# Kernel tuning notes

Hardware: AMD Instinct MI355X
Metric: run time of the kernel (lower is better)

## Reference

```python
import jax, jax.numpy as jnp
import numpy as np
import math

B, S, E = 2, 2048, 1024
NH, NKV, HD = 16, 4, 64
GATE_CH = 12

def _rope(x, cos, sin):
    h = x.shape[-1] // 2
    x1, x2 = x[..., :h], x[..., h:]
    return jnp.concatenate((x1 * cos + x2 * sin, x1 * -sin + x2 * cos), axis=-1)

def _rms_norm(x):
    eps = jnp.finfo(x.dtype).eps
    return x * jax.lax.rsqrt(jnp.mean(x * x, axis=-1, keepdims=True) + eps)

def setup_inputs() -> dict:
    key = jax.random.key(0)
    ks = jax.random.split(key, 9)
    x = jax.random.normal(ks[0], (B, S, E), dtype=jnp.float32)
    ve = jax.random.normal(ks[1], (B, S, NKV * HD), dtype=jnp.float32)
    t = jnp.arange(S, dtype=jnp.float32)[:, None]
    inv_freq = 1.0 / (10000.0 ** (jnp.arange(0, HD // 2, dtype=jnp.float32) / (HD // 2)))
    ang = t * inv_freq[None, :]
    cos = jnp.cos(ang)[None, :, None, :]  # (1,S,1,HD//2)
    sin = jnp.sin(ang)[None, :, None, :]
    attn_mask = jnp.tril(jnp.ones((S, S), dtype=bool))[None, None]  # causal (1,1,S,S)
    sc = 0.02
    Wq = jax.random.normal(ks[2], (NH * HD, E), dtype=jnp.float32) * sc
    Wk = jax.random.normal(ks[3], (NKV * HD, E), dtype=jnp.float32) * sc
    Wv = jax.random.normal(ks[4], (NKV * HD, E), dtype=jnp.float32) * sc
    Wproj = jax.random.normal(ks[5], (E, E), dtype=jnp.float32) * sc
    Wgate = jax.random.normal(ks[6], (NKV, GATE_CH), dtype=jnp.float32) * sc
    return {"x": x, "ve": ve, "cos": cos, "sin": sin, "attn_mask": attn_mask,
            "Wq": Wq, "Wk": Wk, "Wv": Wv, "Wproj": Wproj, "Wgate": Wgate}

def reference(x, ve, cos, sin, attn_mask, Wq, Wk, Wv, Wproj, Wgate):
    b, s, _ = x.shape
    q = (x @ Wq.T).reshape(b, s, NH, HD)
    k = (x @ Wk.T).reshape(b, s, NKV, HD)
    v = (x @ Wv.T).reshape(b, s, NKV, HD)
    # value-embedding gating
    gate = 3.0 * jax.nn.sigmoid(x[..., :GATE_CH] @ Wgate.T)  # (b,s,NKV)
    v = v + gate[..., None] * ve.reshape(b, s, NKV, HD)
    # RoPE + QK-RMSNorm
    q = _rms_norm(_rope(q, cos, sin)) * 1.2
    k = _rms_norm(_rope(k, cos, sin)) * 1.2
    # GQA: repeat KV heads
    rep = NH // NKV
    k = jnp.repeat(k, rep, axis=2)
    v = jnp.repeat(v, rep, axis=2)
    q = q.transpose(0, 2, 1, 3)  # (b,h,s,d)
    k = k.transpose(0, 2, 1, 3)
    v = v.transpose(0, 2, 1, 3)
    scores = jnp.einsum('bhqd,bhkd->bhqk', q, k) / math.sqrt(HD)
    scores = jnp.where(attn_mask, scores, jnp.finfo(scores.dtype).min)
    attn = jax.nn.softmax(scores, axis=-1)
    y = jnp.einsum('bhqk,bhkd->bhqd', attn, v)
    y = y.transpose(0, 2, 1, 3).reshape(b, s, NH * HD)
    return y @ Wproj.T
```

## Files before the change

kernel.cpp:

```cpp
#include <hip/hip_runtime.h>
#include <hip/hip_bf16.h>
#include <math.h>

typedef short bf16x8 __attribute__((ext_vector_type(8)));
typedef float f32x4 __attribute__((ext_vector_type(4)));

#define LROW 72

__device__ __forceinline__ unsigned short f2bf(float f) {
  union { float f; unsigned int u; } v; v.f = f;
  unsigned int u = v.u;
  unsigned int r = (u + 0x7fffu + ((u >> 16) & 1u)) >> 16;
  return (unsigned short)r;
}
__device__ __forceinline__ float bf2f(unsigned short u) {
  return __uint_as_float((unsigned)u << 16);
}

#if __has_builtin(__builtin_amdgcn_global_load_lds)
#define HAVE_GLD 1
__device__ __forceinline__ void gld16(const void* g, void* l) {
  __builtin_amdgcn_global_load_lds(
      (const __attribute__((address_space(1))) unsigned int*)g,
      (__attribute__((address_space(3))) unsigned int*)l, 16, 0, 0);
}
#else
#define HAVE_GLD 0
#endif

__global__ __launch_bounds__(256) void cvt_all_kernel(const float* __restrict__ x,
                                                      const float* __restrict__ Wq,
                                                      const float* __restrict__ Wk,
                                                      const float* __restrict__ Wv,
                                                      const float* __restrict__ Wproj,
                                                      unsigned short* __restrict__ xb,
                                                      unsigned short* __restrict__ wqkv,
                                                      unsigned short* __restrict__ wpj) {
  int blk = blockIdx.x;
  const float* src;
  unsigned short* dst;
  if (blk < 4096)      { src = x + (size_t)blk * 1024;            dst = xb + (size_t)blk * 1024; }
  else if (blk < 5120) { src = Wq + (size_t)(blk - 4096) * 1024;  dst = wqkv + (size_t)(blk - 4096) * 1024; }
  else if (blk < 5376) { src = Wk + (size_t)(blk - 5120) * 1024;  dst = wqkv + (size_t)(blk - 4096) * 1024; }
  else if (blk < 5632) { src = Wv + (size_t)(blk - 5376) * 1024;  dst = wqkv + (size_t)(blk - 4096) * 1024; }
  else                 { src = Wproj + (size_t)(blk - 5632) * 1024; dst = wpj + (size_t)(blk - 5632) * 1024; }
  int i = threadIdx.x;
  float4 v = ((const float4*)src)[i];
  ushort4 o;
  o.x = f2bf(v.x); o.y = f2bf(v.y); o.z = f2bf(v.z); o.w = f2bf(v.w);
  ((ushort4*)dst)[i] = o;
}

__global__ __launch_bounds__(256) void gemm_qkv_kernel(const unsigned short* __restrict__ A,
                                                       const unsigned short* __restrict__ B,
                                                       const float* __restrict__ ve,
                                                       const float* __restrict__ cosb,
                                                       const float* __restrict__ sinb,
                                                       const float* __restrict__ wgate,
                                                       unsigned short* __restrict__ Q,
                                                       unsigned short* __restrict__ Kd,
                                                       unsigned short* __restrict__ Vt) {
  __shared__ unsigned short As[64 * 64];
  __shared__ unsigned short Bs[128 * 64];
  __shared__ float gLDS[128];
  const int K = 1024;
  int wg = blockIdx.x;
  int swz = (wg & 7) * 96 + (wg >> 3);
  int n0 = (swz % 12) * 128;
  int m0 = (swz / 12) * 64;
  int tid = threadIdx.x;
  int wave = tid >> 6, lane = tid & 63, l15 = lane & 15, quad = lane >> 4;
  int wm = (wave >> 1) * 32, wn = (wave & 1) * 64;
  if (n0 >= 1280 && tid < 128) {
    int rl = tid & 63, khl = tid >> 6;
    int kh = ((n0 >> 6) - 20) + khl;
    float dot = 0.f;
#pragma unroll
    for (int jj = 0; jj < 12; jj++)
      dot += bf2f(A[(size_t)(m0 + rl) * 1024 + jj]) * wgate[kh * 12 + jj];
    gLDS[khl * 64 + rl] = 3.0f / (1.0f + __expf(-dot));
  }
  f32x4 acc[2][4];
#pragma unroll
  for (int i = 0; i < 2; i++)
#pragma unroll
    for (int j = 0; j < 4; j++) acc[i][j] = (f32x4){0.f, 0.f, 0.f, 0.f};
  int srow = lane >> 3;
  int scol = ((lane & 7) ^ srow) * 8;
  for (int k0 = 0; k0 < K; k0 += 64) {
    __syncthreads();
#if HAVE_GLD
#pragma unroll
    for (int j = 0; j < 2; j++) {
      int row = wave * 16 + j * 8;
      gld16(A + (size_t)(m0 + row + srow) * K + k0 + scol, As + row * 64 + lane * 8);
    }
#pragma unroll
    for (int j = 0; j < 4; j++) {
      int row = wave * 32 + j * 8;
      gld16(B + (size_t)(n0 + row + srow) * K + k0 + scol, Bs + row * 64 + lane * 8);
    }
#else
#pragma unroll
    for (int j = 0; j < 2; j++) {
      int row = wave * 16 + j * 8;
      *(float4*)(As + row * 64 + lane * 8) = *(const float4*)(A + (size_t)(m0 + row + srow) * K + k0 + scol);
    }
#pragma unroll
    for (int j = 0; j < 4; j++) {
      int row = wave * 32 + j * 8;
      *(float4*)(Bs + row * 64 + lane * 8) = *(const float4*)(B + (size_t)(n0 + row + srow) * K + k0 + scol);
    }
#endif
    __syncthreads();
#pragma unroll
    for (int s = 0; s < 2; s++) {
      bf16x8 af[2], bf[4];
#pragma unroll
      for (int i = 0; i < 2; i++)
        af[i] = *(const bf16x8*)(As + (wm + i * 16 + l15) * 64 + (((s * 4 + quad) ^ (l15 & 7)) * 8));
#pragma unroll
      for (int j = 0; j < 4; j++)
        bf[j] = *(const bf16x8*)(Bs + (wn + j * 16 + l15) * 64 + (((s * 4 + quad) ^ (l15 & 7)) * 8));
#pragma unroll
      for (int i = 0; i < 2; i++)
#pragma unroll
        for (int j = 0; j < 4; j++)
          acc[i][j] = __builtin_amdgcn_mfma_f32_16x16x32_bf16(af[i], bf[j], acc[i][j], 0, 0, 0);
    }
  }
  int hs = (n0 + wn) >> 6;
  if (hs < 20) {
    bool isq = hs < 16;
    float postscale = isq ? 0.216404256f : 1.2f;
#pragma unroll
    for (int i = 0; i < 2; i++) {
#pragma unroll
      for (int r = 0; r < 4; r++) {
        int row = m0 + wm + i * 16 + quad * 4 + r;
        int s = row & 2047, b = row >> 11;
        float c0 = cosb[s * 32 + l15],      s0 = sinb[s * 32 + l15];
        float c1 = cosb[s * 32 + 16 + l15], s1 = sinb[s * 32 + 16 + l15];
        float v0 = acc[i][0][r], v1 = acc[i][1][r], v2 = acc[i][2][r], v3 = acc[i][3][r];
        float n0v = fmaf(v0, c0,  v2 * s0);
        float n1v = fmaf(v1, c1,  v3 * s1);
        float n2v = fmaf(v2, c0, -v0 * s0);
        float n3v = fmaf(v3, c1, -v1 * s1);
        float ss = (n0v * n0v + n1v * n1v) + (n2v * n2v + n3v * n3v);
        ss += __shfl_xor(ss, 1, 64); ss += __shfl_xor(ss, 2, 64);
        ss += __shfl_xor(ss, 4, 64); ss += __shfl_xor(ss, 8, 64);
        float sc = rsqrtf(ss * (1.0f / 64.0f) + 1.1920929e-07f) * postscale;
        unsigned short* dp = isq ? Q + ((size_t)(b * 16 + hs) * 2048 + s) * 64
                                 : Kd + ((size_t)(b * 4 + hs - 16) * 2048 + s) * 64;
        dp[l15]      = f2bf(n0v * sc);
        dp[16 + l15] = f2bf(n1v * sc);
        dp[32 + l15] = f2bf(n2v * sc);
        dp[48 + l15] = f2bf(n3v * sc);
      }
    }
  } else {
    int kh = hs - 20;
#pragma unroll
    for (int i = 0; i < 2; i++) {
#pragma unroll
      for (int r = 0; r < 4; r++) {
        int rl = wm + i * 16 + quad * 4 + r;
        int row = m0 + rl, s = row & 2047, b = row >> 11;
        float g = gLDS[(wave & 1) * 64 + rl];
        const float* vep = ve + (size_t)row * 256 + kh * 64;
        unsigned short* vp = Vt + ((size_t)(b * 4 + kh) * 64) * 2048 + s;
#pragma unroll
        for (int j = 0; j < 4; j++) {
          float vv = fmaf(g, vep[j * 16 + l15], acc[i][j][r]);
          vp[(size_t)(j * 16 + l15) * 2048] = f2bf(vv);
        }
      }
    }
  }
}

__global__ __launch_bounds__(256) void flash_kernel(const unsigned short* __restrict__ Q,
                                                    const unsigned short* __restrict__ K,
                                                    const unsigned short* __restrict__ Vt,
                                                    unsigned short* __restrict__ Y) {
  __shared__ unsigned short Ks[64 * 64];
  __shared__ unsigned short Vs[64 * 64];
  __shared__ unsigned short Ps[4 * 16 * LROW];
  int wg = blockIdx.x;
  int qt = 31 - (wg >> 5);
  int hbb = wg & 31;
  int h = hbb & 15;
  int b = hbb >> 4;
  int hb = b * 16 + h;
  int kh = h >> 2;
  int tid = threadIdx.x, wave = tid >> 6, lane = tid & 63, l15 = lane & 15, quad = lane >> 4;
  int l7 = l15 & 7;
  const unsigned short* Kg = K + (size_t)(b * 4 + kh) * 2048 * 64;
  const unsigned short* Vg = Vt + (size_t)(b * 4 + kh) * 64 * 2048;
  unsigned short* Pw = Ps + wave * 16 * LROW;
  int row0 = tid >> 3, col8 = (tid & 7) * 8;
  int dchunk = (((tid & 7) ^ (row0 & 7)) * 8);

  int NT = qt + 1;
  int q0 = qt * 64;
  const unsigned short* Qp = Q + (((size_t)hb * 2048) + q0 + wave * 16 + l15) * 64;
  bf16x8 qf0 = *(const bf16x8*)(Qp + quad * 8);
  bf16x8 qf1 = *(const bf16x8*)(Qp + 32 + quad * 8);
  f32x4 acc[4];
#pragma unroll
  for (int i = 0; i < 4; i++) acc[i] = (f32x4){0.f, 0.f, 0.f, 0.f};
  float l_lane = 0.f;

  {
    float4 pk0 = *(const float4*)(Kg + (size_t)row0 * 64 + col8);
    float4 pk1 = *(const float4*)(Kg + (size_t)(row0 + 32) * 64 + col8);
    float4 pv0 = *(const float4*)(Vg + (size_t)row0 * 2048 + col8);
    float4 pv1 = *(const float4*)(Vg + (size_t)(row0 + 32) * 2048 + col8);

    for (int kt = 0; kt < NT; kt++) {
      int k0 = kt * 64;
      __syncthreads();
      *(float4*)(Ks + row0 * 64 + dchunk) = pk0;
      *(float4*)(Ks + (row0 + 32) * 64 + dchunk) = pk1;
      *(float4*)(Vs + row0 * 64 + dchunk) = pv0;
      *(float4*)(Vs + (row0 + 32) * 64 + dchunk) = pv1;
      if (kt + 1 < NT) {
        int kn = k0 + 64;
        pk0 = *(const float4*)(Kg + (size_t)(kn + row0) * 64 + col8);
        pk1 = *(const float4*)(Kg + (size_t)(kn + row0 + 32) * 64 + col8);
        pv0 = *(const float4*)(Vg + (size_t)row0 * 2048 + kn + col8);
        pv1 = *(const float4*)(Vg + (size_t)(row0 + 32) * 2048 + kn + col8);
      }
      __syncthreads();

      f32x4 sv[4];
      __builtin_amdgcn_s_setprio(1);
#pragma unroll
      for (int mt = 0; mt < 4; mt++) {
        sv[mt] = (f32x4){0.f, 0.f, 0.f, 0.f};
        bf16x8 k0f = *(const bf16x8*)(Ks + (mt * 16 + l15) * 64 + ((quad ^ l7) * 8));
        sv[mt] = __builtin_amdgcn_mfma_f32_16x16x32_bf16(k0f, qf0, sv[mt], 0, 0, 0);
        bf16x8 k1f = *(const bf16x8*)(Ks + (mt * 16 + l15) * 64 + (((4 + quad) ^ l7) * 8));
        sv[mt] = __builtin_amdgcn_mfma_f32_16x16x32_bf16(k1f, qf1, sv[mt], 0, 0, 0);
      }
      __builtin_amdgcn_s_setprio(0);
      if (kt == qt) {
        int qg = q0 + wave * 16 + l15;
#pragma unroll
        for (int mt = 0; mt < 4; mt++) {
          int kg = k0 + mt * 16 + quad * 4;
#pragma unroll
          for (int r = 0; r < 4; r++)
            if (kg + r > qg) sv[mt][r] = -1e30f;
        }
      }
#pragma unroll
      for (int mt = 0; mt < 4; mt++) {
        float p0 = __builtin_amdgcn_exp2f(sv[mt][0]);
        float p1 = __builtin_amdgcn_exp2f(sv[mt][1]);
        float p2 = __builtin_amdgcn_exp2f(sv[mt][2]);
        float p3 = __builtin_amdgcn_exp2f(sv[mt][3]);
        l_lane += (p0 + p1) + (p2 + p3);
        unsigned int lo = __builtin_amdgcn_perm(__float_as_uint(p1), __float_as_uint(p0), 0x07060302u);
        unsigned int hi = __builtin_amdgcn_perm(__float_as_uint(p3), __float_as_uint(p2), 0x07060302u);
        *(uint2*)(Pw + l15 * LROW + mt * 16 + quad * 4) = make_uint2(lo, hi);
      }
      __builtin_amdgcn_s_setprio(1);
#pragma unroll
      for (int step = 0; step < 2; step++) {
        bf16x8 pa = *(const bf16x8*)(Pw + l15 * LROW + step * 32 + quad * 8);
#pragma unroll
        for (int nt = 0; nt < 4; nt++) {
          bf16x8 vb = *(const bf16x8*)(Vs + (nt * 16 + l15) * 64 + (((step * 4 + quad) ^ l7) * 8));
          acc[nt] = __builtin_amdgcn_mfma_f32_16x16x32_bf16(pa, vb, acc[nt], 0, 0, 0);
        }
      }
      __builtin_amdgcn_s_setprio(0);
    }
  }
  l_lane += __shfl_xor(l_lane, 16, 64);
  l_lane += __shfl_xor(l_lane, 32, 64);

#pragma unroll
  for (int r = 0; r < 4; r++) {
    float inv = 1.0f / __shfl(l_lane, quad * 4 + r, 16);
    int qrow = q0 + wave * 16 + quad * 4 + r;
    unsigned short* yp = Y + ((size_t)(b * 2048 + qrow) * 1024) + h * 64;
#pragma unroll
    for (int nt = 0; nt < 4; nt++)
      yp[nt * 16 + l15] = f2bf(acc[nt][r] * inv);
  }
}

__global__ __launch_bounds__(256) void gemm_proj_kernel(const unsigned short* __restrict__ A,
                                                        const unsigned short* __restrict__ B,
                                                        float* __restrict__ C) {
  __shared__ unsigned short As[128 * 64];
  __shared__ unsigned short Bs[64 * 64];
  const int K = 1024, N = 1024;
  int wg = blockIdx.x;
  int swz = (wg & 7) * 64 + (wg >> 3);
  int n0 = (swz & 15) * 64;
  int m0 = (swz >> 4) * 128;
  int tid = threadIdx.x;
  int wave = tid >> 6, lane = tid & 63, l15 = lane & 15, quad = lane >> 4;
  int wm = (wave >> 1) * 64, wn = (wave & 1) * 32;
  f32x4 acc[4][2];
#pragma unroll
  for (int i = 0; i < 4; i++)
#pragma unroll
    for (int j = 0; j < 2; j++) acc[i][j] = (f32x4){0.f, 0.f, 0.f, 0.f};
  int srow = lane >> 3;
  int scol = ((lane & 7) ^ srow) * 8;
  for (int k0 = 0; k0 < K; k0 += 64) {
    __syncthreads();
#if HAVE_GLD
#pragma unroll
    for (int j = 0; j < 4; j++) {
      int row = wave * 32 + j * 8;
      gld16(A + (size_t)(m0 + row + srow) * K + k0 + scol, As + row * 64 + lane * 8);
    }
#pragma unroll
    for (int j = 0; j < 2; j++) {
      int row = wave * 16 + j * 8;
      gld16(B + (size_t)(n0 + row + srow) * K + k0 + scol, Bs + row * 64 + lane * 8);
    }
#else
#pragma unroll
    for (int j = 0; j < 4; j++) {
      int row = wave * 32 + j * 8;
      *(float4*)(As + row * 64 + lane * 8) = *(const float4*)(A + (size_t)(m0 + row + srow) * K + k0 + scol);
    }
#pragma unroll
    for (int j = 0; j < 2; j++) {
      int row = wave * 16 + j * 8;
      *(float4*)(Bs + row * 64 + lane * 8) = *(const float4*)(B + (size_t)(n0 + row + srow) * K + k0 + scol);
    }
#endif
    __syncthreads();
#pragma unroll
    for (int s = 0; s < 2; s++) {
      bf16x8 af[4], bf[2];
#pragma unroll
      for (int i = 0; i < 4; i++)
        af[i] = *(const bf16x8*)(As + (wm + i * 16 + l15) * 64 + (((s * 4 + quad) ^ (l15 & 7)) * 8));
#pragma unroll
      for (int j = 0; j < 2; j++)
        bf[j] = *(const bf16x8*)(Bs + (wn + j * 16 + l15) * 64 + (((s * 4 + quad) ^ (l15 & 7)) * 8));
#pragma unroll
      for (int i = 0; i < 4; i++)
#pragma unroll
        for (int j = 0; j < 2; j++)
          acc[i][j] = __builtin_amdgcn_mfma_f32_16x16x32_bf16(af[i], bf[j], acc[i][j], 0, 0, 0);
    }
  }
#pragma unroll
  for (int i = 0; i < 4; i++)
#pragma unroll
    for (int j = 0; j < 2; j++)
#pragma unroll
      for (int r = 0; r < 4; r++)
        C[(size_t)(m0 + wm + i * 16 + quad * 4 + r) * N + n0 + wn + j * 16 + l15] = acc[i][j][r];
}

extern "C" void kernel_launch(void* const* d_in, const int* in_sizes, int n_in,
                              void* d_out, int out_size, void* d_ws, size_t ws_size,
                              hipStream_t stream) {
  const float* x     = (const float*)d_in[0];
  const float* ve    = (const float*)d_in[1];
  const float* cosb  = (const float*)d_in[2];
  const float* sinb  = (const float*)d_in[3];
  const float* Wq    = (const float*)d_in[5];
  const float* Wk    = (const float*)d_in[6];
  const float* Wv    = (const float*)d_in[7];
  const float* Wproj = (const float*)d_in[8];
  const float* Wgate = (const float*)d_in[9];
  float* out = (float*)d_out;
  char* ws = (char*)d_ws;

  size_t o = 0;
  unsigned short* xb   = (unsigned short*)(ws + o); o += (size_t)4096 * 1024 * 2;
  unsigned short* wqkv = (unsigned short*)(ws + o); o += (size_t)1536 * 1024 * 2;
  unsigned short* wpj  = (unsigned short*)(ws + o); o += (size_t)1024 * 1024 * 2;
  unsigned short* Qb   = (unsigned short*)(ws + o); o += (size_t)2 * 16 * 2048 * 64 * 2;
  unsigned short* Kb   = (unsigned short*)(ws + o); o += (size_t)2 * 4 * 2048 * 64 * 2;
  unsigned short* Vb   = (unsigned short*)(ws + o); o += (size_t)2 * 4 * 2048 * 64 * 2;
  unsigned short* Yb   = (unsigned short*)(ws + o); o += (size_t)4096 * 1024 * 2;

  hipLaunchKernelGGL(cvt_all_kernel, dim3(6656), dim3(256), 0, stream,
                     x, Wq, Wk, Wv, Wproj, xb, wqkv, wpj);
  hipLaunchKernelGGL(gemm_qkv_kernel, dim3(768), dim3(256), 0, stream,
                     xb, wqkv, ve, cosb, sinb, Wgate, Qb, Kb, Vb);
  hipLaunchKernelGGL(flash_kernel, dim3(1024), dim3(256), 0, stream,
                     Qb, Kb, Vb, Yb);
  hipLaunchKernelGGL(gemm_proj_kernel, dim3(512), dim3(256), 0, stream, Yb, wpj, out);
}
```

Baseline: 168.5 us.

## Stage 128-key KV tiles per barrier pair and swizzle P buffer

The flash kernel now loads 128-key K/V tiles into shared memory per iteration and processes them as two 64-key halves, which halves the number of barrier pairs and global prefetch rounds. The padded P buffer is replaced with an XOR-swizzled 64-wide layout to cut LDS use while avoiding bank conflicts. The V-producing epilogue now writes four consecutive sequence positions as one ushort4 store instead of scalar stores. In exchange, LDS per block roughly doubles for K/V and more prefetch registers are held, which may reduce occupancy, and the causal diagonal can leave half of the last tile unused.

```diff
diff --git a/kernel.cpp b/kernel.cpp
--- a/kernel.cpp
+++ b/kernel.cpp
@@ -4,8 +4,6 @@
 
 typedef short bf16x8 __attribute__((ext_vector_type(8)));
 typedef float f32x4 __attribute__((ext_vector_type(4)));
-
-#define LROW 72
 
 __device__ __forceinline__ unsigned short f2bf(float f) {
   union { float f; unsigned int u; } v; v.f = f;
@@ -162,18 +160,21 @@
     int kh = hs - 20;
 #pragma unroll
     for (int i = 0; i < 2; i++) {
-#pragma unroll
-      for (int r = 0; r < 4; r++) {
-        int rl = wm + i * 16 + quad * 4 + r;
-        int row = m0 + rl, s = row & 2047, b = row >> 11;
-        float g = gLDS[(wave & 1) * 64 + rl];
-        const float* vep = ve + (size_t)row * 256 + kh * 64;
-        unsigned short* vp = Vt + ((size_t)(b * 4 + kh) * 64) * 2048 + s;
-#pragma unroll
-        for (int j = 0; j < 4; j++) {
-          float vv = fmaf(g, vep[j * 16 + l15], acc[i][j][r]);
-          vp[(size_t)(j * 16 + l15) * 2048] = f2bf(vv);
-        }
+      int row0 = m0 + wm + i * 16 + quad * 4;
+      int s0 = row0 & 2047, b0 = row0 >> 11;
+      float g0 = gLDS[(wave & 1) * 64 + wm + i * 16 + quad * 4 + 0];
+      float g1 = gLDS[(wave & 1) * 64 + wm + i * 16 + quad * 4 + 1];
+      float g2 = gLDS[(wave & 1) * 64 + wm + i * 16 + quad * 4 + 2];
+      float g3 = gLDS[(wave & 1) * 64 + wm + i * 16 + quad * 4 + 3];
+#pragma unroll
+      for (int j = 0; j < 4; j++) {
+        int d = j * 16 + l15;
+        ushort4 o4;
+        o4.x = f2bf(fmaf(g0, ve[(size_t)(row0 + 0) * 256 + kh * 64 + d], acc[i][j][0]));
+        o4.y = f2bf(fmaf(g1, ve[(size_t)(row0 + 1) * 256 + kh * 64 + d], acc[i][j][1]));
+        o4.z = f2bf(fmaf(g2, ve[(size_t)(row0 + 2) * 256 + kh * 64 + d], acc[i][j][2]));
+        o4.w = f2bf(fmaf(g3, ve[(size_t)(row0 + 3) * 256 + kh * 64 + d], acc[i][j][3]));
+        *(ushort4*)(Vt + ((size_t)(b0 * 4 + kh) * 64 + d) * 2048 + s0) = o4;
       }
     }
   }
@@ -183,9 +184,9 @@
                                                     const unsigned short* __restrict__ K,
                                                     const unsigned short* __restrict__ Vt,
                                                     unsigned short* __restrict__ Y) {
-  __shared__ unsigned short Ks[64 * 64];
-  __shared__ unsigned short Vs[64 * 64];
-  __shared__ unsigned short Ps[4 * 16 * LROW];
+  __shared__ unsigned short Ks[128 * 64];
+  __shared__ unsigned short Vs[64 * 128];
+  __shared__ unsigned short Ps[4 * 16 * 64];
   int wg = blockIdx.x;
   int qt = 31 - (wg >> 5);
   int hbb = wg & 31;
@@ -195,13 +196,18 @@
   int kh = h >> 2;
   int tid = threadIdx.x, wave = tid >> 6, lane = tid & 63, l15 = lane & 15, quad = lane >> 4;
   int l7 = l15 & 7;
+  int pm = l15 & 14;
   const unsigned short* Kg = K + (size_t)(b * 4 + kh) * 2048 * 64;
   const unsigned short* Vg = Vt + (size_t)(b * 4 + kh) * 64 * 2048;
-  unsigned short* Pw = Ps + wave * 16 * LROW;
-  int row0 = tid >> 3, col8 = (tid & 7) * 8;
-  int dchunk = (((tid & 7) ^ (row0 & 7)) * 8);
-
-  int NT = qt + 1;
+  unsigned short* Pw = Ps + wave * 16 * 64;
+  int krow = tid >> 3, kcol = (tid & 7) * 8;
+  int dchK = ((tid & 7) ^ (krow & 7)) * 8;
+  int vrow = tid >> 4, vc = tid & 15;
+  int vcol = vc * 8;
+  int dchV = ((vc & 8) | ((vc & 7) ^ (vrow & 7))) * 8;
+
+  int NT64 = qt + 1;
+  int NT128 = (qt + 2) >> 1;
   int q0 = qt * 64;
   const unsigned short* Qp = Q + (((size_t)hb * 2048) + q0 + wave * 16 + l15) * 64;
   bf16x8 qf0 = *(const bf16x8*)(Qp + quad * 8);
@@ -211,40 +217,48 @@
   for (int i = 0; i < 4; i++) acc[i] = (f32x4){0.f, 0.f, 0.f, 0.f};
   float l_lane = 0.f;
 
-  {
-    float4 pk0 = *(const float4*)(Kg + (size_t)row0 * 64 + col8);
-    float4 pk1 = *(const float4*)(Kg + (size_t)(row0 + 32) * 64 + col8);
-    float4 pv0 = *(const float4*)(Vg + (size_t)row0 * 2048 + col8);
-    float4 pv1 = *(const float4*)(Vg + (size_t)(row0 + 32) * 2048 + col8);
-
-    for (int kt = 0; kt < NT; kt++) {
-      int k0 = kt * 64;
-      __syncthreads();
-      *(float4*)(Ks + row0 * 64 + dchunk) = pk0;
-      *(float4*)(Ks + (row0 + 32) * 64 + dchunk) = pk1;
-      *(float4*)(Vs + row0 * 64 + dchunk) = pv0;
-      *(float4*)(Vs + (row0 + 32) * 64 + dchunk) = pv1;
-      if (kt + 1 < NT) {
-        int kn = k0 + 64;
-        pk0 = *(const float4*)(Kg + (size_t)(kn + row0) * 64 + col8);
-        pk1 = *(const float4*)(Kg + (size_t)(kn + row0 + 32) * 64 + col8);
-        pv0 = *(const float4*)(Vg + (size_t)row0 * 2048 + kn + col8);
-        pv1 = *(const float4*)(Vg + (size_t)(row0 + 32) * 2048 + kn + col8);
-      }
-      __syncthreads();
-
+  float4 pk[4], pv[4];
+#pragma unroll
+  for (int m = 0; m < 4; m++) {
+    pk[m] = *(const float4*)(Kg + (size_t)(krow + m * 32) * 64 + kcol);
+    pv[m] = *(const float4*)(Vg + (size_t)(vrow + m * 16) * 2048 + vcol);
+  }
+
+  for (int kt = 0; kt < NT128; kt++) {
+    __syncthreads();
+#pragma unroll
+    for (int m = 0; m < 4; m++) {
+      *(float4*)(Ks + (krow + m * 32) * 64 + dchK) = pk[m];
+      *(float4*)(Vs + (vrow + m * 16) * 128 + dchV) = pv[m];
+    }
+    if (kt + 1 < NT128) {
+      int kn = (kt + 1) * 128;
+#pragma unroll
+      for (int m = 0; m < 4; m++) {
+        pk[m] = *(const float4*)(Kg + (size_t)(kn + krow + m * 32) * 64 + kcol);
+        pv[m] = *(const float4*)(Vg + (size_t)(vrow + m * 16) * 2048 + kn + vcol);
+      }
+    }
+    __syncthreads();
+
+#pragma unroll
+    for (int half = 0; half < 2; half++) {
+      int h64 = kt * 2 + half;
+      if (h64 >= NT64) break;
+      int k0 = h64 * 64;
+      const unsigned short* Kh = Ks + half * 64 * 64;
       f32x4 sv[4];
       __builtin_amdgcn_s_setprio(1);
 #pragma unroll
       for (int mt = 0; mt < 4; mt++) {
         sv[mt] = (f32x4){0.f, 0.f, 0.f, 0.f};
-        bf16x8 k0f = *(const bf16x8*)(Ks + (mt * 16 + l15) * 64 + ((quad ^ l7) * 8));
+        bf16x8 k0f = *(const bf16x8*)(Kh + (mt * 16 + l15) * 64 + ((quad ^ l7) * 8));
         sv[mt] = __builtin_amdgcn_mfma_f32_16x16x32_bf16(k0f, qf0, sv[mt], 0, 0, 0);
-        bf16x8 k1f = *(const bf16x8*)(Ks + (mt * 16 + l15) * 64 + (((4 + quad) ^ l7) * 8));
+        bf16x8 k1f = *(const bf16x8*)(Kh + (mt * 16 + l15) * 64 + (((4 + quad) ^ l7) * 8));
         sv[mt] = __builtin_amdgcn_mfma_f32_16x16x32_bf16(k1f, qf1, sv[mt], 0, 0, 0);
       }
       __builtin_amdgcn_s_setprio(0);
-      if (kt == qt) {
+      if (h64 == qt) {
         int qg = q0 + wave * 16 + l15;
 #pragma unroll
         for (int mt = 0; mt < 4; mt++) {
@@ -263,15 +277,16 @@
         l_lane += (p0 + p1) + (p2 + p3);
         unsigned int lo = __builtin_amdgcn_perm(__float_as_uint(p1), __float_as_uint(p0), 0x07060302u);
         unsigned int hi = __builtin_amdgcn_perm(__float_as_uint(p3), __float_as_uint(p2), 0x07060302u);
-        *(uint2*)(Pw + l15 * LROW + mt * 16 + quad * 4) = make_uint2(lo, hi);
+        *(uint2*)(Pw + l15 * 64 + (((mt * 4 + quad) ^ pm) << 2)) = make_uint2(lo, hi);
       }
       __builtin_amdgcn_s_setprio(1);
 #pragma unroll
       for (int step = 0; step < 2; step++) {
-        bf16x8 pa = *(const bf16x8*)(Pw + l15 * LROW + step * 32 + quad * 8);
+        bf16x8 pa = *(const bf16x8*)(Pw + l15 * 64 + (((step * 8 + quad * 2) ^ pm) << 2));
 #pragma unroll
         for (int nt = 0; nt < 4; nt++) {
-          bf16x8 vb = *(const bf16x8*)(Vs + (nt * 16 + l15) * 64 + (((step * 4 + quad) ^ l7) * 8));
+          bf16x8 vb = *(const bf16x8*)(Vs + (nt * 16 + l15) * 128 +
+                                       (half * 8 + ((step * 4 + quad) ^ l7)) * 8);
           acc[nt] = __builtin_amdgcn_mfma_f32_16x16x32_bf16(pa, vb, acc[nt], 0, 0, 0);
         }
       }
```

After: 233.7 us. 1.39x slower.
